# Kernel optimization log

Measured on AMD Instinct MI355X. Metric: run time of the kernel, lower is better.

The kernel has to match this reference:

```python
import jax, jax.numpy as jnp
import numpy as np

B, P, N, E, H, D = 8, 1000, 1000, 128, 8, 16  # batch, pomo, nodes, embed, heads, qkv_dim
SQRT_E = float(np.sqrt(E))
CLIP = 10.0
INV_SQRT_D = 1.0 / float(np.sqrt(D))


def _heads(x):
    # [b, n, H*D] -> [b, H, n, D]
    b, n, _ = x.shape
    return x.reshape(b, n, H, D).transpose(0, 2, 1, 3)


def _mha(q, k, v, ninf_mask):
    # q: [b,H,P,D], k/v: [b,H,N,D], ninf_mask: [b,P,N]
    score = jnp.einsum('bhnd,bhsd->bhns', q, k) * INV_SQRT_D
    score = score + ninf_mask[:, None, :, :]
    w = jax.nn.softmax(score, axis=-1)
    out = jnp.einsum('bhns,bhsd->bhnd', w, v)
    return out.transpose(0, 2, 1, 3).reshape(q.shape[0], q.shape[2], H * D)


def setup_inputs() -> dict:
    key = jax.random.key(0)
    ks = jax.random.split(key, 16)
    s = 0.02
    return {
        'encoded_last_node': jax.random.normal(ks[0], (B, P, E), jnp.float32),
        'attr': jax.random.normal(ks[1], (B, P, 4), jnp.float32),
        'encoded_nodes': jax.random.normal(ks[2], (B, N, E), jnp.float32),
        'ninf_mask': jnp.zeros((B, P, N), jnp.float32),
        'Wq_shared': jax.random.normal(ks[3], (E + 4, H * D), jnp.float32) * s,
        'Wk_shared': jax.random.normal(ks[4], (E, H * D), jnp.float32) * s,
        'Wv_shared': jax.random.normal(ks[5], (E, H * D), jnp.float32) * s,
        'Wq_task': jax.random.normal(ks[6], (E + 4, H * D), jnp.float32) * s,
        'Wk_task': jax.random.normal(ks[7], (E, H * D), jnp.float32) * s,
        'Wv_task': jax.random.normal(ks[8], (E, H * D), jnp.float32) * s,
        'Wc_shared': jax.random.normal(ks[9], (H * D, E), jnp.float32) * s,
        'bc_shared': jnp.zeros((E,), jnp.float32),
        'Wc_task': jax.random.normal(ks[10], (H * D, E), jnp.float32) * s,
        'bc_task': jnp.zeros((E,), jnp.float32),
        'Wg': jax.random.normal(ks[11], (E + 4, E), jnp.float32) * s,
        'bg': jnp.zeros((E,), jnp.float32),
    }


def reference(encoded_last_node, attr, encoded_nodes, ninf_mask,
              Wq_shared, Wk_shared, Wv_shared, Wq_task, Wk_task, Wv_task,
              Wc_shared, bc_shared, Wc_task, bc_task, Wg, bg):
    # set_kv
    k_shared = _heads(encoded_nodes @ Wk_shared)
    v_shared = _heads(encoded_nodes @ Wv_shared)
    k_task = _heads(encoded_nodes @ Wk_task)
    v_task = _heads(encoded_nodes @ Wv_task)

    # decoder forward
    input_cat = jnp.concatenate([encoded_last_node, attr], axis=2)  # [B,P,E+4]
    q_shared = _heads(input_cat @ Wq_shared)
    q_task = _heads(input_cat @ Wq_task)

    out_shared = _mha(q_shared, k_shared, v_shared, ninf_mask) @ Wc_shared + bc_shared
    out_task = _mha(q_task, k_task, v_task, ninf_mask) @ Wc_task + bc_task

    gate = jax.nn.sigmoid(input_cat @ Wg + bg)
    gated_out = gate * out_shared + (1.0 - gate) * out_task  # [B,P,E]

    # pointer scores against single-head key (encoded_nodes)
    score = jnp.einsum('bpe,bne->bpn', gated_out, encoded_nodes) / SQRT_E
    score_clipped = CLIP * jnp.tanh(score)
    probs = jax.nn.softmax(score_clipped + ninf_mask, axis=2)
    return probs
```

## Files before the change

### kernel.cpp

```cpp
#include <hip/hip_runtime.h>
#include <math.h>

#define BB 8
#define PP 1000
#define NN 1000
#define EE 128
#define HH 8
#define DD 16

#define INV_SQRT_E 0.08838834764831845f
#define LOG2E      1.4426950408889634f
#define QSCALE     0.3606737602222409f

typedef short short8_t __attribute__((ext_vector_type(8)));
typedef float f32x4    __attribute__((ext_vector_type(4)));
typedef float f32x16   __attribute__((ext_vector_type(16)));
typedef __bf16 bf16x4  __attribute__((ext_vector_type(4)));
typedef __bf16 bf16x8  __attribute__((ext_vector_type(8)));

__device__ __forceinline__ float sigmoid_fast(float x) {
    return 1.f / (1.f + __expf(-x));
}
__device__ __forceinline__ float tanh_fast(float x) {
    x = fminf(fmaxf(x, -15.f), 15.f);
    float e = __expf(2.f * x);
    return (e - 1.f) / (e + 1.f);
}

__device__ __forceinline__ f32x4 mfma16(short8_t a, short8_t b, f32x4 c) {
    return __builtin_amdgcn_mfma_f32_16x16x32_bf16(a, b, c, 0, 0, 0);
}
__device__ __forceinline__ f32x16 mfma32(short8_t a, short8_t b, f32x16 c) {
    return __builtin_amdgcn_mfma_f32_32x32x16_bf16(a, b, c, 0, 0, 0);
}

__device__ __forceinline__ float sum16(float x) {
    int v;
    v = __builtin_amdgcn_update_dpp(0, __builtin_bit_cast(int, x), 0xB1, 0xF, 0xF, true);
    x += __builtin_bit_cast(float, v);
    v = __builtin_amdgcn_update_dpp(0, __builtin_bit_cast(int, x), 0x4E, 0xF, 0xF, true);
    x += __builtin_bit_cast(float, v);
    v = __builtin_amdgcn_update_dpp(0, __builtin_bit_cast(int, x), 0x141, 0xF, 0xF, true);
    x += __builtin_bit_cast(float, v);
    v = __builtin_amdgcn_update_dpp(0, __builtin_bit_cast(int, x), 0x140, 0xF, 0xF, true);
    x += __builtin_bit_cast(float, v);
    return x;
}

__global__ __launch_bounds__(256) void prep_kernel(
    const float* __restrict__ mask, const float* __restrict__ nodes,
    const float* __restrict__ eln,  const float* __restrict__ attr,
    const float* __restrict__ Wk_s, const float* __restrict__ Wv_s,
    const float* __restrict__ Wk_t, const float* __restrict__ Wv_t,
    const float* __restrict__ Wq_s, const float* __restrict__ Wq_t,
    const float* __restrict__ Wg,   const float* __restrict__ Wc_s,
    const float* __restrict__ Wc_t,
    __bf16* __restrict__ emaskb, __bf16* __restrict__ nodesb,
    __bf16* __restrict__ inb, __bf16* __restrict__ Wtb)
{
    const int bx = blockIdx.x;
    __shared__ float tile[32][129];
    if (bx < 1954) {
        int base = (bx * 256 + threadIdx.x) * 16;
        if (base < 8000000) {
            float4 v0 = *(const float4*)&mask[base];
            float4 v1 = *(const float4*)&mask[base + 4];
            float4 v2 = *(const float4*)&mask[base + 8];
            float4 v3 = *(const float4*)&mask[base + 12];
            bf16x4 p0 = { (__bf16)(v0.x * LOG2E), (__bf16)(v0.y * LOG2E),
                          (__bf16)(v0.z * LOG2E), (__bf16)(v0.w * LOG2E) };
            bf16x4 p1 = { (__bf16)(v1.x * LOG2E), (__bf16)(v1.y * LOG2E),
                          (__bf16)(v1.z * LOG2E), (__bf16)(v1.w * LOG2E) };
            bf16x4 p2 = { (__bf16)(v2.x * LOG2E), (__bf16)(v2.y * LOG2E),
                          (__bf16)(v2.z * LOG2E), (__bf16)(v2.w * LOG2E) };
            bf16x4 p3 = { (__bf16)(v3.x * LOG2E), (__bf16)(v3.y * LOG2E),
                          (__bf16)(v3.z * LOG2E), (__bf16)(v3.w * LOG2E) };
            *(bf16x4*)&emaskb[base]      = p0;
            *(bf16x4*)&emaskb[base + 4]  = p1;
            *(bf16x4*)&emaskb[base + 8]  = p2;
            *(bf16x4*)&emaskb[base + 12] = p3;
        }
    } else if (bx < 2204) {
        int base = ((bx - 1954) * 256 + threadIdx.x) * 16;
        float4 v0 = *(const float4*)&nodes[base];
        float4 v1 = *(const float4*)&nodes[base + 4];
        float4 v2 = *(const float4*)&nodes[base + 8];
        float4 v3 = *(const float4*)&nodes[base + 12];
        bf16x4 p0 = { (__bf16)v0.x, (__bf16)v0.y, (__bf16)v0.z, (__bf16)v0.w };
        bf16x4 p1 = { (__bf16)v1.x, (__bf16)v1.y, (__bf16)v1.z, (__bf16)v1.w };
        bf16x4 p2 = { (__bf16)v2.x, (__bf16)v2.y, (__bf16)v2.z, (__bf16)v2.w };
        bf16x4 p3 = { (__bf16)v3.x, (__bf16)v3.y, (__bf16)v3.z, (__bf16)v3.w };
        *(bf16x4*)&nodesb[base]      = p0;
        *(bf16x4*)&nodesb[base + 4]  = p1;
        *(bf16x4*)&nodesb[base + 8]  = p2;
        *(bf16x4*)&nodesb[base + 12] = p3;
    } else if (bx < 2829) {
        int t = (bx - 2204) * 256 + threadIdx.x;
        int row = t / 20, seg = t - row * 20;
        bf16x8 o = {};
        if (seg < 16) {
            const float* p = &eln[(size_t)row * 128 + seg * 8];
            float4 a = *(const float4*)p, b = *(const float4*)(p + 4);
            o = bf16x8{ (__bf16)a.x, (__bf16)a.y, (__bf16)a.z, (__bf16)a.w,
                        (__bf16)b.x, (__bf16)b.y, (__bf16)b.z, (__bf16)b.w };
        } else if (seg == 16) {
            float4 a = *(const float4*)&attr[(size_t)row * 4];
            o = bf16x8{ (__bf16)a.x, (__bf16)a.y, (__bf16)a.z, (__bf16)a.w,
                        (__bf16)0.f, (__bf16)0.f, (__bf16)0.f, (__bf16)0.f };
        }
        *(bf16x8*)&inb[(size_t)row * 160 + seg * 8] = o;
    } else {
        int idx = bx - 2829;
        int m = idx / 5, kt = idx - m * 5;
        const float* srcs[9] = {Wk_s, Wv_s, Wk_t, Wv_t, Wq_s, Wq_t, Wg, Wc_s, Wc_t};
        const int   srcKs[9] = {128, 128, 128, 128, 132, 132, 132, 128, 128};
        const int   kpads[9] = {128, 128, 128, 128, 160, 160, 160, 128, 128};
        const size_t offs[9] = {0, 16384, 32768, 49152, 65536, 86016, 106496, 126976, 143360};
        const int kp = kpads[m];
        if (kt * 32 >= kp) return;
        const float* src = srcs[m];
        const int sK = srcKs[m];
        const size_t off = offs[m];
        const int tid = threadIdx.x;
        for (int j = tid; j < 32 * 128; j += 256) {
            int kk = j >> 7, n = j & 127;
            int k = kt * 32 + kk;
            tile[kk][n] = (k < sK) ? src[(size_t)k * 128 + n] : 0.f;
        }
        __syncthreads();
        for (int j = tid; j < 32 * 128; j += 256) {
            int n = j >> 5, kk = j & 31;
            Wtb[off + (size_t)n * kp + kt * 32 + kk] = (__bf16)tile[kk][n];
        }
    }
}

template<int NC>
__device__ __forceinline__ void proj_body(
    const __bf16* __restrict__ A, const __bf16* __restrict__ W,
    f32x4 acc[8], int r0, int quad, int lq)
{
    const int K = NC * 32;
    short8_t aF[NC];
    #pragma unroll
    for (int c = 0; c < NC; ++c)
        aF[c] = *(const short8_t*)&A[(size_t)(r0 + lq) * K + c * 32 + quad * 8];
    #pragma unroll
    for (int nt = 0; nt < 8; ++nt) {
        acc[nt] = f32x4{0.f, 0.f, 0.f, 0.f};
        #pragma unroll
        for (int c = 0; c < NC; ++c) {
            short8_t bF = *(const short8_t*)&W[(size_t)(nt * 16 + lq) * K + c * 32 + quad * 8];
            acc[nt] = mfma16(aF[c], bF, acc[nt]);
        }
    }
}

__global__ __launch_bounds__(256) void proj_mfma_kernel(
    const __bf16* __restrict__ nodesb, const __bf16* __restrict__ inb,
    const __bf16* __restrict__ Wtb,
    __bf16* __restrict__ kb_s, __bf16* __restrict__ vt_s,
    __bf16* __restrict__ kb_t, __bf16* __restrict__ vt_t,
    __bf16* __restrict__ qb_s, __bf16* __restrict__ qb_t)
{
    const int wsel = blockIdx.y;
    const int wave = threadIdx.x >> 6, lane = threadIdx.x & 63;
    const int quad = lane >> 4, lq = lane & 15;
    const int r0 = blockIdx.x * 64 + wave * 16;

    f32x4 acc[8];
    if (wsel < 4) {
        proj_body<4>(nodesb, Wtb + (size_t)wsel * 16384, acc, r0, quad, lq);
    } else {
        proj_body<5>(inb, Wtb + 65536 + (size_t)(wsel - 4) * 20480, acc, r0, quad, lq);
    }

    if (wsel == 0 || wsel == 2) {
        __bf16* O = (wsel == 0) ? kb_s : kb_t;
        #pragma unroll
        for (int r = 0; r < 4; ++r) {
            int m = r0 + quad * 4 + r;
            int b = m / 1000, n = m - b * 1000;
            #pragma unroll
            for (int nt = 0; nt < 8; ++nt)
                O[(((size_t)(b * 8 + nt) * 1000 + n) << 4) + lq] = (__bf16)acc[nt][r];
        }
    } else if (wsel == 4 || wsel == 5) {
        __bf16* O = (wsel == 4) ? qb_s : qb_t;
        #pragma unroll
        for (int r = 0; r < 4; ++r) {
            int m = r0 + quad * 4 + r;
            int b = m / 1000, n = m - b * 1000;
            #pragma unroll
            for (int nt = 0; nt < 8; ++nt)
                O[(((size_t)(b * 8 + nt) * 1000 + n) << 4) + lq] =
                    (__bf16)(acc[nt][r] * QSCALE);
        }
    } else {
        __bf16* O = (wsel == 1) ? vt_s : vt_t;
        #pragma unroll
        for (int r = 0; r < 4; ++r) {
            int m = r0 + quad * 4 + r;
            int b = m / 1000, n = m - b * 1000;
            int rr = n & 31;
            int pos = (n & ~31) + ((rr < 16) ? (rr << 1) : (((rr - 16) << 1) | 1));
            #pragma unroll
            for (int nt = 0; nt < 8; ++nt)
                O[(((size_t)(b * 8 + nt) * 16 + lq) << 10) + pos] = (__bf16)acc[nt][r];
        }
    }
}

__global__ __launch_bounds__(256) void attn_mfma_kernel(
    const __bf16* __restrict__ qb_s, const __bf16* __restrict__ qb_t,
    const __bf16* __restrict__ kb_s, const __bf16* __restrict__ kb_t,
    const __bf16* __restrict__ vt_s, const __bf16* __restrict__ vt_t,
    const __bf16* __restrict__ emaskb,
    __bf16* __restrict__ att_s, __bf16* __restrict__ att_t)
{
    const int b    = blockIdx.z;
    const int wave = threadIdx.x >> 6;
    const int combo = blockIdx.y * 4 + wave;
    const int br = combo & 1;
    const int h  = combo >> 1;
    const __bf16* Q  = br ? qb_t : qb_s;
    const __bf16* K  = br ? kb_t : kb_s;
    const __bf16* Vt = br ? vt_t : vt_s;
    __bf16* O        = br ? att_t : att_s;
    const int lane = threadIdx.x & 63;
    const int quad = lane >> 4, lq = lane & 15;
    const int col  = lane & 31;
    const int half = lane >> 5;
    const int bh = b * HH + h;
    const int p0 = blockIdx.x * 32;

    __shared__ __align__(16) __bf16 S[4][2][32][40];

    int pq = p0 + col; if (pq > 999) pq = 999;
    short8_t qB = *(const short8_t*)&Q[(((size_t)bh * 1000 + pq) << 4) + half * 8];
    const __bf16* mp = emaskb + ((size_t)b * 1000 + pq) * 1000 + 4 * half;

    short8_t onesB = { (short)0x3F80, (short)0x3F80, (short)0x3F80, (short)0x3F80,
                       (short)0x3F80, (short)0x3F80, (short)0x3F80, (short)0x3F80 };

    f32x4 o[2] = { {0.f,0.f,0.f,0.f}, {0.f,0.f,0.f,0.f} };
    f32x4 l[2] = { {0.f,0.f,0.f,0.f}, {0.f,0.f,0.f,0.f} };

    short8_t kAc = *(const short8_t*)&K[(((size_t)bh * 1000 + col) << 4) + half * 8];
    short8_t vBc = *(const short8_t*)&Vt[(((size_t)bh * 16 + lq) << 10) + quad * 8];

    #pragma unroll 2
    for (int n0 = 0; n0 < 992; n0 += 32) {
        const int par = (n0 >> 5) & 1;
        int nk = n0 + 32 + col; if (nk > 999) nk = 999;
        short8_t kAn = *(const short8_t*)&K[(((size_t)bh * 1000 + nk) << 4) + half * 8];
        short8_t vBn = *(const short8_t*)&Vt[(((size_t)bh * 16 + lq) << 10) + n0 + 32 + quad * 8];
        bf16x4 m2[4];
        #pragma unroll
        for (int g = 0; g < 4; ++g)
            m2[g] = *(const bf16x4*)&mp[n0 + 8 * g];

        f32x16 s = mfma32(kAc, qB, f32x16{});

        #pragma unroll
        for (int g = 0; g < 4; ++g) {
            bf16x4 pk;
            #pragma unroll
            for (int j = 0; j < 4; ++j)
                pk[j] = (__bf16)__builtin_amdgcn_exp2f(s[4 * g + j] + (float)m2[g][j]);
            *(bf16x4*)&S[wave][par][col][8 * g + 4 * half] = pk;
        }

        #pragma unroll
        for (int t = 0; t < 2; ++t) {
            short8_t aP = *(const short8_t*)&S[wave][par][t * 16 + lq][quad * 8];
            o[t] = mfma16(aP, vBc, o[t]);
            l[t] = mfma16(aP, onesB, l[t]);
        }
        kAc = kAn; vBc = vBn;
    }

    {
        bf16x4 m2t = *(const bf16x4*)&mp[992];
        f32x16 s = mfma32(kAc, qB, f32x16{});
        bf16x4 pk0;
        #pragma unroll
        for (int j = 0; j < 4; ++j)
            pk0[j] = (__bf16)__builtin_amdgcn_exp2f(s[j] + (float)m2t[j]);
        *(bf16x4*)&S[wave][1][col][4 * half] = pk0;
        bf16x4 z = {};
        #pragma unroll
        for (int g = 1; g < 4; ++g)
            *(bf16x4*)&S[wave][1][col][8 * g + 4 * half] = z;

        #pragma unroll
        for (int t = 0; t < 2; ++t) {
            short8_t aP = *(const short8_t*)&S[wave][1][t * 16 + lq][quad * 8];
            o[t] = mfma16(aP, vBc, o[t]);
            l[t] = mfma16(aP, onesB, l[t]);
        }
    }

    #pragma unroll
    for (int t = 0; t < 2; ++t)
        #pragma unroll
        for (int r = 0; r < 4; ++r) {
            int p = p0 + t * 16 + quad * 4 + r;
            if (p < 1000)
                O[((size_t)b * 1000 + p) * 128 + h * 16 + lq] = (__bf16)(o[t][r] / l[t][r]);
        }
}

__global__ __launch_bounds__(256) void combine_mfma_kernel(
    const __bf16* __restrict__ att_s, const __bf16* __restrict__ att_t,
    const __bf16* __restrict__ inb, const __bf16* __restrict__ Wtb,
    const float* __restrict__ bc_s, const float* __restrict__ bc_t,
    const float* __restrict__ bg, __bf16* __restrict__ gatedb)
{
    const int wave = threadIdx.x >> 6, lane = threadIdx.x & 63;
    const int quad = lane >> 4, lq = lane & 15;
    const int r0 = blockIdx.x * 64 + wave * 16;
    const int nt = blockIdx.y;
    const __bf16* Wgp = Wtb + 106496;
    const __bf16* Ws  = Wtb + 126976;
    const __bf16* Wt  = Wtb + 143360;

    short8_t aS[4], aT[4], aG[5];
    #pragma unroll
    for (int c = 0; c < 4; ++c) {
        aS[c] = *(const short8_t*)&att_s[(size_t)(r0 + lq) * 128 + c * 32 + quad * 8];
        aT[c] = *(const short8_t*)&att_t[(size_t)(r0 + lq) * 128 + c * 32 + quad * 8];
    }
    #pragma unroll
    for (int c = 0; c < 5; ++c)
        aG[c] = *(const short8_t*)&inb[(size_t)(r0 + lq) * 160 + c * 32 + quad * 8];

    f32x4 accS = {0.f,0.f,0.f,0.f}, accT = accS, accG = accS;
    #pragma unroll
    for (int c = 0; c < 4; ++c) {
        short8_t bS = *(const short8_t*)&Ws[(size_t)(nt * 16 + lq) * 128 + c * 32 + quad * 8];
        short8_t bT = *(const short8_t*)&Wt[(size_t)(nt * 16 + lq) * 128 + c * 32 + quad * 8];
        accS = mfma16(aS[c], bS, accS);
        accT = mfma16(aT[c], bT, accT);
    }
    #pragma unroll
    for (int c = 0; c < 5; ++c) {
        short8_t bG = *(const short8_t*)&Wgp[(size_t)(nt * 16 + lq) * 160 + c * 32 + quad * 8];
        accG = mfma16(aG[c], bG, accG);
    }
    int f = nt * 16 + lq;
    float b1 = bc_s[f], b2 = bc_t[f], b3 = bg[f];
    #pragma unroll
    for (int r = 0; r < 4; ++r) {
        int m = r0 + quad * 4 + r;
        float g = sigmoid_fast(accG[r] + b3);
        float val = g * (accS[r] + b1) + (1.f - g) * (accT[r] + b2);
        gatedb[(size_t)m * 128 + f] = (__bf16)val;
    }
}

__global__ __launch_bounds__(512) void pointer_softmax_kernel(
    const __bf16* __restrict__ gb, const __bf16* __restrict__ nb,
    const __bf16* __restrict__ emaskb, float* __restrict__ out)
{
    const int b    = blockIdx.y;
    const int p0   = blockIdx.x * 16;
    const int wave = threadIdx.x >> 6;
    const int lane = threadIdx.x & 63;
    const int quad = lane >> 4, lq = lane & 15;

    __shared__ float Spart[8][16];

    short8_t aF[4];
    {
        int pp = p0 + lq; if (pp > 999) pp = 999;
        const __bf16* arow = gb + (((size_t)b * 1000 + pp) << 7) + quad * 8;
        #pragma unroll
        for (int kc = 0; kc < 4; ++kc) aF[kc] = *(const short8_t*)&arow[kc * 32];
    }

    float ev[8][4];
    float psum[4] = {0.f, 0.f, 0.f, 0.f};

    #pragma unroll
    for (int i = 0; i < 8; ++i) {
        const int nt = i * 8 + wave;
        const int nn = nt * 16 + lq;
        const bool nv = nn < 1000;
        int nc = nv ? nn : 999;
        const __bf16* brow = nb + (((size_t)b * 1000 + nc) << 7) + quad * 8;
        f32x4 acc = {0.f, 0.f, 0.f, 0.f};
        #pragma unroll
        for (int kc = 0; kc < 4; ++kc) {
            short8_t bF = *(const short8_t*)&brow[kc * 32];
            acc = mfma16(aF[kc], bF, acc);
        }
        #pragma unroll
        for (int r = 0; r < 4; ++r) {
            int p = p0 + quad * 4 + r;
            bool v = nv && (p < 1000);
            size_t midx = v ? ((size_t)b * 1000 + p) * 1000 + nn : 0;
            float m2 = (float)emaskb[midx];
            float sc = 10.f * tanh_fast(acc[r] * INV_SQRT_E);
            float ee = v ? __builtin_amdgcn_exp2f(sc * LOG2E + m2) : 0.f;
            ev[i][r] = ee;
            psum[r] += ee;
        }
    }

    #pragma unroll
    for (int r = 0; r < 4; ++r) psum[r] = sum16(psum[r]);
    if (lq == 0) {
        #pragma unroll
        for (int r = 0; r < 4; ++r) Spart[wave][quad * 4 + r] = psum[r];
    }
    __syncthreads();
    float inv[4];
    #pragma unroll
    for (int r = 0; r < 4; ++r) {
        int row = quad * 4 + r;
        float s = 0.f;
        #pragma unroll
        for (int wv = 0; wv < 8; ++wv) s += Spart[wv][row];
        inv[r] = 1.f / s;
    }

    #pragma unroll
    for (int i = 0; i < 8; ++i) {
        const int nt = i * 8 + wave;
        const int nn = nt * 16 + lq;
        if (nn < 1000) {
            #pragma unroll
            for (int r = 0; r < 4; ++r) {
                int p = p0 + quad * 4 + r;
                if (p < 1000)
                    out[((size_t)b * 1000 + p) * 1000 + nn] = ev[i][r] * inv[r];
            }
        }
    }
}

extern "C" void kernel_launch(void* const* d_in, const int* in_sizes, int n_in,
                              void* d_out, int out_size, void* d_ws, size_t ws_size,
                              hipStream_t stream)
{
    const float* eln   = (const float*)d_in[0];
    const float* attr  = (const float*)d_in[1];
    const float* nodes = (const float*)d_in[2];
    const float* mask  = (const float*)d_in[3];
    const float* Wq_s  = (const float*)d_in[4];
    const float* Wk_s  = (const float*)d_in[5];
    const float* Wv_s  = (const float*)d_in[6];
    const float* Wq_t  = (const float*)d_in[7];
    const float* Wk_t  = (const float*)d_in[8];
    const float* Wv_t  = (const float*)d_in[9];
    const float* Wc_s  = (const float*)d_in[10];
    const float* bc_s  = (const float*)d_in[11];
    const float* Wc_t  = (const float*)d_in[12];
    const float* bc_t  = (const float*)d_in[13];
    const float* Wg    = (const float*)d_in[14];
    const float* bg    = (const float*)d_in[15];
    float* out = (float*)d_out;

    char* w = (char*)d_ws;
    const size_t KB_SZ = (size_t)64 * 1000 * 16 * 2;
    const size_t VT_SZ = (size_t)64 * 16 * 1024 * 2;
    const size_t H_SZ  = (size_t)8000 * 128 * 2;
    const size_t IN_SZ = (size_t)8000 * 160 * 2;
    const size_t EM_SZ = (size_t)8000 * 1000 * 2;
    __bf16* kb_s  = (__bf16*)w;           w += KB_SZ;
    __bf16* kb_t  = (__bf16*)w;           w += KB_SZ;
    __bf16* qb_s  = (__bf16*)w;           w += KB_SZ;
    __bf16* qb_t  = (__bf16*)w;           w += KB_SZ;
    __bf16* vt_s  = (__bf16*)w;           w += VT_SZ;
    __bf16* vt_t  = (__bf16*)w;           w += VT_SZ;
    __bf16* att_s = (__bf16*)w;           w += H_SZ;
    __bf16* att_t = (__bf16*)w;           w += H_SZ;
    __bf16* gatedb = (__bf16*)w;          w += H_SZ;
    __bf16* nodesb = (__bf16*)w;          w += H_SZ;
    __bf16* inb    = (__bf16*)w;          w += IN_SZ;
    __bf16* emaskb = (__bf16*)w;          w += EM_SZ;
    __bf16* Wtb    = (__bf16*)w;          w += 320000;

    hipMemsetAsync(vt_s, 0, 2 * VT_SZ, stream);

    prep_kernel<<<dim3(2874), 256, 0, stream>>>(
        mask, nodes, eln, attr, Wk_s, Wv_s, Wk_t, Wv_t, Wq_s, Wq_t, Wg,
        Wc_s, Wc_t, emaskb, nodesb, inb, Wtb);
    proj_mfma_kernel<<<dim3(125, 6), 256, 0, stream>>>(
        nodesb, inb, Wtb, kb_s, vt_s, kb_t, vt_t, qb_s, qb_t);
    attn_mfma_kernel<<<dim3(32, 4, 8), 256, 0, stream>>>(
        qb_s, qb_t, kb_s, kb_t, vt_s, vt_t, emaskb, att_s, att_t);
    combine_mfma_kernel<<<dim3(125, 8), 256, 0, stream>>>(
        att_s, att_t, inb, Wtb, bc_s, bc_t, bg, gatedb);
    pointer_softmax_kernel<<<dim3(63, 8), 512, 0, stream>>>(
        gatedb, nodesb, emaskb, out);
}
```

Measured before the change: 228.4 us.

## Process shared and task attention branches in one wave to reuse mask loads

Each attention wave now computes both the shared and task branches for one head, so the bf16 mask tile is loaded and converted once per branch pair instead of twice. It also interleaves the two branches' MFMA and exp work for more ILP, and halves the grid in y. The cost is higher register and LDS use per wave and fewer blocks, which may reduce occupancy. The prep kernel edits only roll repeated statements into loops.

```diff
diff --git a/kernel.cpp b/kernel.cpp
--- a/kernel.cpp
+++ b/kernel.cpp
@@ -63,37 +63,22 @@
     if (bx < 1954) {
         int base = (bx * 256 + threadIdx.x) * 16;
         if (base < 8000000) {
-            float4 v0 = *(const float4*)&mask[base];
-            float4 v1 = *(const float4*)&mask[base + 4];
-            float4 v2 = *(const float4*)&mask[base + 8];
-            float4 v3 = *(const float4*)&mask[base + 12];
-            bf16x4 p0 = { (__bf16)(v0.x * LOG2E), (__bf16)(v0.y * LOG2E),
-                          (__bf16)(v0.z * LOG2E), (__bf16)(v0.w * LOG2E) };
-            bf16x4 p1 = { (__bf16)(v1.x * LOG2E), (__bf16)(v1.y * LOG2E),
-                          (__bf16)(v1.z * LOG2E), (__bf16)(v1.w * LOG2E) };
-            bf16x4 p2 = { (__bf16)(v2.x * LOG2E), (__bf16)(v2.y * LOG2E),
-                          (__bf16)(v2.z * LOG2E), (__bf16)(v2.w * LOG2E) };
-            bf16x4 p3 = { (__bf16)(v3.x * LOG2E), (__bf16)(v3.y * LOG2E),
-                          (__bf16)(v3.z * LOG2E), (__bf16)(v3.w * LOG2E) };
-            *(bf16x4*)&emaskb[base]      = p0;
-            *(bf16x4*)&emaskb[base + 4]  = p1;
-            *(bf16x4*)&emaskb[base + 8]  = p2;
-            *(bf16x4*)&emaskb[base + 12] = p3;
+            #pragma unroll
+            for (int q = 0; q < 4; ++q) {
+                float4 v = *(const float4*)&mask[base + q * 4];
+                bf16x4 p = { (__bf16)(v.x * LOG2E), (__bf16)(v.y * LOG2E),
+                             (__bf16)(v.z * LOG2E), (__bf16)(v.w * LOG2E) };
+                *(bf16x4*)&emaskb[base + q * 4] = p;
+            }
         }
     } else if (bx < 2204) {
         int base = ((bx - 1954) * 256 + threadIdx.x) * 16;
-        float4 v0 = *(const float4*)&nodes[base];
-        float4 v1 = *(const float4*)&nodes[base + 4];
-        float4 v2 = *(const float4*)&nodes[base + 8];
-        float4 v3 = *(const float4*)&nodes[base + 12];
-        bf16x4 p0 = { (__bf16)v0.x, (__bf16)v0.y, (__bf16)v0.z, (__bf16)v0.w };
-        bf16x4 p1 = { (__bf16)v1.x, (__bf16)v1.y, (__bf16)v1.z, (__bf16)v1.w };
-        bf16x4 p2 = { (__bf16)v2.x, (__bf16)v2.y, (__bf16)v2.z, (__bf16)v2.w };
-        bf16x4 p3 = { (__bf16)v3.x, (__bf16)v3.y, (__bf16)v3.z, (__bf16)v3.w };
-        *(bf16x4*)&nodesb[base]      = p0;
-        *(bf16x4*)&nodesb[base + 4]  = p1;
-        *(bf16x4*)&nodesb[base + 8]  = p2;
-        *(bf16x4*)&nodesb[base + 12] = p3;
+        #pragma unroll
+        for (int q = 0; q < 4; ++q) {
+            float4 v = *(const float4*)&nodes[base + q * 4];
+            bf16x4 p = { (__bf16)v.x, (__bf16)v.y, (__bf16)v.z, (__bf16)v.w };
+            *(bf16x4*)&nodesb[base + q * 4] = p;
+        }
     } else if (bx < 2829) {
         int t = (bx - 2204) * 256 + threadIdx.x;
         int row = t / 20, seg = t - row * 20;
@@ -220,13 +205,7 @@
 {
     const int b    = blockIdx.z;
     const int wave = threadIdx.x >> 6;
-    const int combo = blockIdx.y * 4 + wave;
-    const int br = combo & 1;
-    const int h  = combo >> 1;
-    const __bf16* Q  = br ? qb_t : qb_s;
-    const __bf16* K  = br ? kb_t : kb_s;
-    const __bf16* Vt = br ? vt_t : vt_s;
-    __bf16* O        = br ? att_t : att_s;
+    const int h    = blockIdx.y * 4 + wave;
     const int lane = threadIdx.x & 63;
     const int quad = lane >> 4, lq = lane & 15;
     const int col  = lane & 31;
@@ -234,70 +213,127 @@
     const int bh = b * HH + h;
     const int p0 = blockIdx.x * 32;
 
-    __shared__ __align__(16) __bf16 S[4][2][32][40];
+    __shared__ __align__(16) __bf16 S[4][2][2][32][40];
 
     int pq = p0 + col; if (pq > 999) pq = 999;
-    short8_t qB = *(const short8_t*)&Q[(((size_t)bh * 1000 + pq) << 4) + half * 8];
+    short8_t qS = *(const short8_t*)&qb_s[(((size_t)bh * 1000 + pq) << 4) + half * 8];
+    short8_t qT = *(const short8_t*)&qb_t[(((size_t)bh * 1000 + pq) << 4) + half * 8];
     const __bf16* mp = emaskb + ((size_t)b * 1000 + pq) * 1000 + 4 * half;
 
     short8_t onesB = { (short)0x3F80, (short)0x3F80, (short)0x3F80, (short)0x3F80,
                        (short)0x3F80, (short)0x3F80, (short)0x3F80, (short)0x3F80 };
 
-    f32x4 o[2] = { {0.f,0.f,0.f,0.f}, {0.f,0.f,0.f,0.f} };
-    f32x4 l[2] = { {0.f,0.f,0.f,0.f}, {0.f,0.f,0.f,0.f} };
-
-    short8_t kAc = *(const short8_t*)&K[(((size_t)bh * 1000 + col) << 4) + half * 8];
-    short8_t vBc = *(const short8_t*)&Vt[(((size_t)bh * 16 + lq) << 10) + quad * 8];
+    f32x4 oS[2] = { {0.f,0.f,0.f,0.f}, {0.f,0.f,0.f,0.f} };
+    f32x4 lS[2] = { {0.f,0.f,0.f,0.f}, {0.f,0.f,0.f,0.f} };
+    f32x4 oT[2] = { {0.f,0.f,0.f,0.f}, {0.f,0.f,0.f,0.f} };
+    f32x4 lT[2] = { {0.f,0.f,0.f,0.f}, {0.f,0.f,0.f,0.f} };
+
+    const size_t kqoff = (((size_t)bh * 1000) << 4) + half * 8;
+    const size_t voff  = (((size_t)bh * 16 + lq) << 10) + quad * 8;
+
+    short8_t kScur = *(const short8_t*)&kb_s[kqoff + ((size_t)col << 4)];
+    short8_t kTcur = *(const short8_t*)&kb_t[kqoff + ((size_t)col << 4)];
+    short8_t vScur = *(const short8_t*)&vt_s[voff];
+    short8_t vTcur = *(const short8_t*)&vt_t[voff];
 
     #pragma unroll 2
     for (int n0 = 0; n0 < 992; n0 += 32) {
         const int par = (n0 >> 5) & 1;
         int nk = n0 + 32 + col; if (nk > 999) nk = 999;
-        short8_t kAn = *(const short8_t*)&K[(((size_t)bh * 1000 + nk) << 4) + half * 8];
-        short8_t vBn = *(const short8_t*)&Vt[(((size_t)bh * 16 + lq) << 10) + n0 + 32 + quad * 8];
+        short8_t kSn = *(const short8_t*)&kb_s[kqoff + ((size_t)nk << 4)];
+        short8_t kTn = *(const short8_t*)&kb_t[kqoff + ((size_t)nk << 4)];
+        short8_t vSn = *(const short8_t*)&vt_s[voff + n0 + 32];
+        short8_t vTn = *(const short8_t*)&vt_t[voff + n0 + 32];
+
         bf16x4 m2[4];
         #pragma unroll
         for (int g = 0; g < 4; ++g)
             m2[g] = *(const bf16x4*)&mp[n0 + 8 * g];
-
-        f32x16 s = mfma32(kAc, qB, f32x16{});
-
+        float mf[16];
+        #pragma unroll
+        for (int g = 0; g < 4; ++g)
+            #pragma unroll
+            for (int j = 0; j < 4; ++j)
+                mf[4 * g + j] = (float)m2[g][j];
+
+        f32x16 sS = mfma32(kScur, qS, f32x16{});
         #pragma unroll
         for (int g = 0; g < 4; ++g) {
             bf16x4 pk;
             #pragma unroll
             for (int j = 0; j < 4; ++j)
-                pk[j] = (__bf16)__builtin_amdgcn_exp2f(s[4 * g + j] + (float)m2[g][j]);
-            *(bf16x4*)&S[wave][par][col][8 * g + 4 * half] = pk;
-        }
+                pk[j] = (__bf16)__builtin_amdgcn_exp2f(sS[4 * g + j] + mf[4 * g + j]);
+            *(bf16x4*)&S[wave][par][0][col][8 * g + 4 * half] = pk;
+        }
+
+        f32x16 sT = mfma32(kTcur, qT, f32x16{});
 
         #pragma unroll
         for (int t = 0; t < 2; ++t) {
-            short8_t aP = *(const short8_t*)&S[wave][par][t * 16 + lq][quad * 8];
-            o[t] = mfma16(aP, vBc, o[t]);
-            l[t] = mfma16(aP, onesB, l[t]);
-        }
-        kAc = kAn; vBc = vBn;
+            short8_t aP = *(const short8_t*)&S[wave][par][0][t * 16 + lq][quad * 8];
+            oS[t] = mfma16(aP, vScur, oS[t]);
+            lS[t] = mfma16(aP, onesB, lS[t]);
+        }
+
+        #pragma unroll
+        for (int g = 0; g < 4; ++g) {
+            bf16x4 pk;
+            #pragma unroll
+            for (int j = 0; j < 4; ++j)
+                pk[j] = (__bf16)__builtin_amdgcn_exp2f(sT[4 * g + j] + mf[4 * g + j]);
+            *(bf16x4*)&S[wave][par][1][col][8 * g + 4 * half] = pk;
+        }
+
+        #pragma unroll
+        for (int t = 0; t < 2; ++t) {
+            short8_t aP = *(const short8_t*)&S[wave][par][1][t * 16 + lq][quad * 8];
+            oT[t] = mfma16(aP, vTcur, oT[t]);
+            lT[t] = mfma16(aP, onesB, lT[t]);
+        }
+
+        kScur = kSn; kTcur = kTn; vScur = vSn; vTcur = vTn;
     }
 
     {
         bf16x4 m2t = *(const bf16x4*)&mp[992];
-        f32x16 s = mfma32(kAc, qB, f32x16{});
-        bf16x4 pk0;
+        float mft[4];
+        #pragma unroll
+        for (int j = 0; j < 4; ++j) mft[j] = (float)m2t[j];
+        bf16x4 z = {};
+
+        f32x16 sS = mfma32(kScur, qS, f32x16{});
+        bf16x4 pkS;
         #pragma unroll
         for (int j = 0; j < 4; ++j)
-            pk0[j] = (__bf16)__builtin_amdgcn_exp2f(s[j] + (float)m2t[j]);
-        *(bf16x4*)&S[wave][1][col][4 * half] = pk0;
-        bf16x4 z = {};
+            pkS[j] = (__bf16)__builtin_amdgcn_exp2f(sS[j] + mft[j]);
+        *(bf16x4*)&S[wave][1][0][col][4 * half] = pkS;
         #pragma unroll
         for (int g = 1; g < 4; ++g)
-            *(bf16x4*)&S[wave][1][col][8 * g + 4 * half] = z;
+            *(bf16x4*)&S[wave][1][0][col][8 * g + 4 * half] = z;
+
+        f32x16 sT = mfma32(kTcur, qT, f32x16{});
 
         #pragma unroll
         for (int t = 0; t < 2; ++t) {
-            short8_t aP = *(const short8_t*)&S[wave][1][t * 16 + lq][quad * 8];
-            o[t] = mfma16(aP, vBc, o[t]);
-            l[t] = mfma16(aP, onesB, l[t]);
+            short8_t aP = *(const short8_t*)&S[wave][1][0][t * 16 + lq][quad * 8];
+            oS[t] = mfma16(aP, vScur, oS[t]);
+            lS[t] = mfma16(aP, onesB, lS[t]);
+        }
+
+        bf16x4 pkT;
+        #pragma unroll
+        for (int j = 0; j < 4; ++j)
+            pkT[j] = (__bf16)__builtin_amdgcn_exp2f(sT[j] + mft[j]);
+        *(bf16x4*)&S[wave][1][1][col][4 * half] = pkT;
+        #pragma unroll
+        for (int g = 1; g < 4; ++g)
+            *(bf16x4*)&S[wave][1][1][col][8 * g + 4 * half] = z;
+
+        #pragma unroll
+        for (int t = 0; t < 2; ++t) {
+            short8_t aP = *(const short8_t*)&S[wave][1][1][t * 16 + lq][quad * 8];
+            oT[t] = mfma16(aP, vTcur, oT[t]);
+            lT[t] = mfma16(aP, onesB, lT[t]);
         }
     }
 
@@ -306,8 +342,11 @@
         #pragma unroll
         for (int r = 0; r < 4; ++r) {
             int p = p0 + t * 16 + quad * 4 + r;
-            if (p < 1000)
-                O[((size_t)b * 1000 + p) * 128 + h * 16 + lq] = (__bf16)(o[t][r] / l[t][r]);
+            if (p < 1000) {
+                size_t oidx = ((size_t)b * 1000 + p) * 128 + h * 16 + lq;
+                att_s[oidx] = (__bf16)(oS[t][r] / lS[t][r]);
+                att_t[oidx] = (__bf16)(oT[t][r] / lT[t][r]);
+            }
         }
 }
 
@@ -489,7 +528,7 @@
         Wc_s, Wc_t, emaskb, nodesb, inb, Wtb);
     proj_mfma_kernel<<<dim3(125, 6), 256, 0, stream>>>(
         nodesb, inb, Wtb, kb_s, vt_s, kb_t, vt_t, qb_s, qb_t);
-    attn_mfma_kernel<<<dim3(32, 4, 8), 256, 0, stream>>>(
+    attn_mfma_kernel<<<dim3(32, 2, 8), 256, 0, stream>>>(
         qb_s, qb_t, kb_s, kb_t, vt_s, vt_t, emaskb, att_s, att_t);
     combine_mfma_kernel<<<dim3(125, 8), 256, 0, stream>>>(
         att_s, att_t, inb, Wtb, bc_s, bc_t, bg, gatedb);
```

Result: no change. 226.8 us (-0.7%).
